# Kernel tuning notes

Measured on AMD Instinct MI355X. Metric: run time of the kernel, lower is better.

## Reference

```python
import jax, jax.numpy as jnp
import numpy as np

KS = 7
HEADS = 8


def _conv1x1(a, w, b):
    # a: (B,Cin,H,W), w: (Cout,Cin), b: (Cout,)
    return jnp.einsum('bchw,oc->bohw', a, w) + b[None, :, None, None]


def _unfold2d(a, ks):
    # a: (B,C,Hp,Wp) -> (B,C,H,W,ks,ks) sliding windows, stride 1
    H = a.shape[2] - ks + 1
    W = a.shape[3] - ks + 1
    ii = jnp.arange(H)[:, None] + jnp.arange(ks)[None, :]  # (H,ks)
    jj = jnp.arange(W)[:, None] + jnp.arange(ks)[None, :]  # (W,ks)
    return a[:, :, ii[:, None, :, None], jj[None, :, None, :]]


def setup_inputs() -> dict:
    key = jax.random.key(0)
    ks = jax.random.split(key, 10)
    B, C, H, W = 4, 128, 56, 56
    x = jax.random.normal(ks[0], (B, C, H, W), dtype=jnp.float32)
    sc = 1.0 / np.sqrt(C)
    q_w = jax.random.normal(ks[1], (C, C), dtype=jnp.float32) * sc
    q_b = jax.random.normal(ks[2], (C,), dtype=jnp.float32) * 0.01
    k_w = jax.random.normal(ks[3], (C, C), dtype=jnp.float32) * sc
    k_b = jax.random.normal(ks[4], (C,), dtype=jnp.float32) * 0.01
    v_w = jax.random.normal(ks[5], (C, C), dtype=jnp.float32) * sc
    v_b = jax.random.normal(ks[6], (C,), dtype=jnp.float32) * 0.01
    rel_h = jax.random.normal(ks[7], (C // 2, KS, 1), dtype=jnp.float32)
    rel_w = jax.random.normal(ks[8], (C // 2, 1, KS), dtype=jnp.float32)
    return {'x': x, 'q_w': q_w, 'q_b': q_b, 'k_w': k_w, 'k_b': k_b,
            'v_w': v_w, 'v_b': v_b, 'rel_h': rel_h, 'rel_w': rel_w}


def reference(x, q_w, q_b, k_w, k_b, v_w, v_b, rel_h, rel_w):
    B, C, H, W = x.shape
    dkh = C // HEADS
    K2 = KS * KS
    pl = (KS - 1) // 2
    pr = KS - 1 - pl
    xp = jnp.pad(x, ((0, 0), (0, 0), (pl, pr), (pl, pr)))

    k = _conv1x1(xp, k_w, k_b)
    v = _conv1x1(xp, v_w, v_b)
    q = _conv1x1(x, q_w, q_b)

    # unfold K/V into (B,C,H,W,KS,KS) then reshape exactly as torch does
    # (this reshape intermixes channel/window axes; replicated faithfully)
    k6 = _unfold2d(k, KS).reshape(B, HEADS, H, W, dkh, K2)
    v6 = _unfold2d(v, KS).reshape(B, HEADS, H, W, dkh, K2)
    q6 = q.reshape(B, HEADS, H, W, dkh, 1)

    # q^T k over the dkh axis -> (B,heads,H,W,KS,KS)
    qk = jnp.einsum('bhxyd,bhxydk->bhxyk', q6[..., 0], k6)
    qk = qk.reshape(B, HEADS, H, W, KS, KS)

    # einsum 'bhxydz,cij->bhxyij' has no shared index: factorizes as
    # (sum over d,z of q) * (sum over c of rel)
    qsum = q6.sum(axis=(4, 5))  # (B,heads,H,W)
    qk = qk + qsum[..., None, None] * rel_h.sum(axis=0)  # (KS,1) broadcast
    qk = qk + qsum[..., None, None] * rel_w.sum(axis=0)  # (1,KS) broadcast

    w = jax.nn.softmax(qk.reshape(B, HEADS, H, W, K2), axis=-1)
    out = jnp.einsum('bhxyk,bhxydk->bhxyd', w, v6)  # (B,heads,H,W,dvh)
    return out.reshape(B, C, H, W)
```

## Files before the change

kernel.cpp:

```cpp
#include <hip/hip_runtime.h>
#include <hip/hip_bf16.h>
#include <math.h>

#define NB    4
#define NC    128
#define NPIX  3136
#define CHW   401408
#define SKS   68

typedef _Float16 f16;
typedef _Float16 f16x8 __attribute__((ext_vector_type(8)));
typedef float f32x4 __attribute__((ext_vector_type(4)));

template <int CTRL, int RM>
__device__ __forceinline__ float dpp_mov(float x, float old) {
    return __int_as_float(__builtin_amdgcn_update_dpp(
        __float_as_int(old), __float_as_int(x), CTRL, RM, 0xf, false));
}
__device__ __forceinline__ float wave_sum(float x) {
    x = x + dpp_mov<0x111, 0xf>(x, 0.f);
    x = x + dpp_mov<0x112, 0xf>(x, 0.f);
    x = x + dpp_mov<0x114, 0xf>(x, 0.f);
    x = x + dpp_mov<0x118, 0xf>(x, 0.f);
    x = x + dpp_mov<0x142, 0xa>(x, 0.f);
    x = x + dpp_mov<0x143, 0xc>(x, 0.f);
    return __int_as_float(__builtin_amdgcn_readlane(__float_as_int(x), 63));
}

__global__ __launch_bounds__(256) void prep_kernel(
    const float* __restrict__ qw, const float* __restrict__ kw,
    const float* __restrict__ vw,
    const float* __restrict__ rel_h, const float* __restrict__ rel_w,
    ushort* __restrict__ pk, float* __restrict__ rb)
{
    int idx = blockIdx.x * 256 + threadIdx.x;
    if (idx < 3 * 32768) {
        int e    = idx & 7;
        int l    = (idx >> 3) & 63;
        int ks   = (idx >> 9) & 3;
        int mt   = (idx >> 11) & 7;
        int prec = (idx >> 14) & 1;
        int mat  = idx >> 15;
        int o = mt * 16 + (l & 15);
        int c = ks * 32 + (l >> 4) * 8 + e;
        const float* src = (mat == 0) ? qw : (mat == 1) ? kw : vw;
        float w = src[o * 128 + c];
        f16 wh = (f16)w;
        f16 v = prec ? (f16)(w - (float)wh) : wh;
        ushort u;
        __builtin_memcpy(&u, &v, 2);
        pk[idx] = u;
    }
    if (idx < 14) {
        const float* src = (idx < 7) ? rel_h : rel_w;
        int off = (idx < 7) ? idx : idx - 7;
        float s = 0.f;
        for (int c = 0; c < 64; ++c) s += src[c * 7 + off];
        rb[idx] = s;
    }
}

__global__ __launch_bounds__(256) void conv_kernel(
    const float* __restrict__ x, const ushort* __restrict__ pk,
    const float* __restrict__ qb, const float* __restrict__ kb,
    const float* __restrict__ vb,
    float* __restrict__ q, float* __restrict__ kbuf, float* __restrict__ vbuf)
{
    __shared__ __align__(16) ushort sh[16 * 136];
    __shared__ __align__(16) ushort sl[16 * 136];
    int bid = blockIdx.x;
    int mat = bid % 3;
    int t2 = bid / 3;
    int tile = t2 % 196;
    int b = t2 / 196;
    int pix0 = tile * 16;
    const float* xb = x + b * CHW + pix0;

    {
        int c = threadIdx.x >> 1;
        int px8 = (threadIdx.x & 1) * 8;
        float4 v0 = *(const float4*)(xb + c * NPIX + px8);
        float4 v1 = *(const float4*)(xb + c * NPIX + px8 + 4);
        float vv[8] = {v0.x, v0.y, v0.z, v0.w, v1.x, v1.y, v1.z, v1.w};
        #pragma unroll
        for (int j = 0; j < 8; ++j) {
            f16 h = (f16)vv[j];
            f16 l = (f16)(vv[j] - (float)h);
            ushort uh, ul;
            __builtin_memcpy(&uh, &h, 2);
            __builtin_memcpy(&ul, &l, 2);
            sh[(px8 + j) * 136 + c] = uh;
            sl[(px8 + j) * 136 + c] = ul;
        }
    }
    __syncthreads();

    int lane = threadIdx.x & 63;
    int wave = threadIdx.x >> 6;
    int px = lane & 15;
    int lg = lane >> 4;

    f16x8 bxh[4], bxl[4];
    #pragma unroll
    for (int ks = 0; ks < 4; ++ks) {
        bxh[ks] = *(const f16x8*)(sh + px * 136 + ks * 32 + lg * 8);
        bxl[ks] = *(const f16x8*)(sl + px * 136 + ks * 32 + lg * 8);
    }

    int mtb = wave * 2;
    const f16x8* PK = (const f16x8*)pk;
    f32x4 acc0 = {0.f, 0.f, 0.f, 0.f};
    f32x4 acc1 = {0.f, 0.f, 0.f, 0.f};
    #pragma unroll
    for (int ks = 0; ks < 4; ++ks) {
        f16x8 wh0 = PK[(((mat * 2 + 0) * 8 + mtb)     * 4 + ks) * 64 + lane];
        f16x8 wh1 = PK[(((mat * 2 + 0) * 8 + mtb + 1) * 4 + ks) * 64 + lane];
        acc0 = __builtin_amdgcn_mfma_f32_16x16x32_f16(wh0, bxh[ks], acc0, 0, 0, 0);
        acc1 = __builtin_amdgcn_mfma_f32_16x16x32_f16(wh1, bxh[ks], acc1, 0, 0, 0);
        acc0 = __builtin_amdgcn_mfma_f32_16x16x32_f16(wh0, bxl[ks], acc0, 0, 0, 0);
        acc1 = __builtin_amdgcn_mfma_f32_16x16x32_f16(wh1, bxl[ks], acc1, 0, 0, 0);
    }
    const float* bias = (mat == 0) ? qb : (mat == 1) ? kb : vb;
    float* dst = ((mat == 0) ? q : (mat == 1) ? kbuf : vbuf)
                 + b * CHW + pix0 + px;
    #pragma unroll
    for (int r = 0; r < 4; ++r) {
        int o0 = mtb * 16 + lg * 4 + r;
        int o1 = o0 + 16;
        dst[o0 * NPIX] = acc0[r] + bias[o0];
        dst[o1 * NPIX] = acc1[r] + bias[o1];
    }
}

__global__ __launch_bounds__(256) void attn_kernel(
    const float* __restrict__ q, const float* __restrict__ kbuf,
    const float* __restrict__ vbuf,
    const float* __restrict__ kb, const float* __restrict__ vb,
    const float* __restrict__ rb, float* __restrict__ out)
{
    __shared__ float sK[20 * SKS];
    __shared__ float sV[21 * SKS];
    __shared__ float sW[4 * 64];
    int bid = blockIdx.x;
    int qpart = bid & 3;
    int bc = bid >> 2;
    int ch = bc & 127;
    const float* qc = q + bc * NPIX + 784 * qpart;
    const float* kc = kbuf + bc * NPIX;
    const float* vc = vbuf + bc * NPIX;
    float* oc = out + bc * NPIX + 784 * qpart;
    float kbias = kb[ch], vbias = vb[ch];
    int qr0 = 14 * qpart;

    for (int i = threadIdx.x; i < 20 * 62; i += 256) {
        int yy = i / 62, xx = i - yy * 62;
        int gy = qr0 + yy - 3;
        int gx = xx - 3;
        bool in = (gy >= 0) && (gy < 56) && (gx >= 0) && (gx < 56);
        int off = in ? gy * 56 + gx : 0;
        float kv = in ? kc[off] : kbias;
        float vv = in ? vc[off] : vbias;
        sK[yy * SKS + xx] = kv;
        sV[yy * SKS + xx] = vv;
    }
    for (int i = threadIdx.x; i < SKS; i += 256) sV[20 * SKS + i] = 0.f;

    int lane = threadIdx.x & 63;
    int wave = threadIdx.x >> 6;
    int k2 = min(lane, 48);
    int di = k2 / 7, dj = k2 - di * 7;
    float rbias = rb[di] + rb[7 + dj];
    int koff = di * SKS + dj;
    int t16 = lane & 15, p = lane >> 4;
    float* sWw = sW + wave * 64;

    float rhM = rb[0], rhm = rb[0];
    #pragma unroll
    for (int i = 1; i < 7; ++i) { rhM = fmaxf(rhM, rb[i]); rhm = fminf(rhm, rb[i]); }
    float rwM = rb[7], rwm = rb[7];
    #pragma unroll
    for (int i = 8; i < 14; ++i) { rwM = fmaxf(rwM, rb[i]); rwm = fminf(rwm, rb[i]); }
    float rdMax = rbias - (rhM + rwM);
    float rdMin = rbias - (rhm + rwm);

    int ul0 = wave * 16;
    int y0 = 0, x0 = ul0;
    float4 p0 = *(const float4*)(qc + ul0);
    float4 p1 = *(const float4*)(qc + ul0 + 4);
    float4 p2 = *(const float4*)(qc + ul0 + 8);
    float4 p3 = *(const float4*)(qc + ul0 + 12);
    __syncthreads();

    for (int gl = wave; gl < 49; gl += 4) {
        float qs = (((p0.x + p0.y) + (p0.z + p0.w)) + ((p1.x + p1.y) + (p1.z + p1.w)))
                 + (((p2.x + p2.y) + (p2.z + p2.w)) + ((p3.x + p3.y) + (p3.z + p3.w)));
        const float* kp = sK + y0 * SKS + x0 + koff;
        int d2 = (x0 == 48) ? (SKS - 48) : 8;
        const float* kp2 = kp + d2;
        float a0, a1;
        a0  = p0.x * kp[0];   a1  = p0.y * kp[1];
        a0 += p0.z * kp[2];   a1 += p0.w * kp[3];
        a0 += p1.x * kp[4];   a1 += p1.y * kp[5];
        a0 += p1.z * kp[6];   a1 += p1.w * kp[7];
        a0 += p2.x * kp2[0];  a1 += p2.y * kp2[1];
        a0 += p2.z * kp2[2];  a1 += p2.w * kp2[3];
        a0 += p3.x * kp2[4];  a1 += p3.y * kp2[5];
        a0 += p3.z * kp2[6];  a1 += p3.w * kp2[7];
        float acc = a0 + a1;

        if (gl + 4 < 49) {
            int un = ul0 + 64;
            p0 = *(const float4*)(qc + un);
            p1 = *(const float4*)(qc + un + 4);
            p2 = *(const float4*)(qc + un + 8);
            p3 = *(const float4*)(qc + un + 12);
        }

        float rd = (qs > 0.f) ? rdMax : rdMin;
        float ex = fmaf(qs, rd, acc);
        float e = (lane < 49) ? __expf(ex) : 0.f;
        float sS = wave_sum(e);
        float wgt = e * __builtin_amdgcn_rcpf(sS);
        sWw[lane] = wgt;

        int u = ul0 + t16;
        int yt = u / 56;
        int xt = u - yt * 56;
        const float* vbase = sV + yt * SKS + xt + p * (2 * SKS);
        const float* wbase = sWw + p * 14;
        float o0 = 0.f, o1 = 0.f;
        #pragma unroll
        for (int j = 0; j < 7; ++j) o0 += wbase[j] * vbase[j];
        #pragma unroll
        for (int j = 0; j < 7; ++j) o1 += wbase[7 + j] * vbase[SKS + j];
        float oacc = o0 + o1;
        oacc += __shfl_xor(oacc, 16);
        oacc += __shfl_xor(oacc, 32);
        if (lane < 16) oc[ul0 + lane] = oacc;

        ul0 += 64;
        x0 += 8; y0 += 1;
        if (x0 >= 56) { x0 -= 56; ++y0; }
    }
}

extern "C" void kernel_launch(void* const* d_in, const int* in_sizes, int n_in,
                              void* d_out, int out_size, void* d_ws, size_t ws_size,
                              hipStream_t stream) {
    const float* x     = (const float*)d_in[0];
    const float* qw    = (const float*)d_in[1];
    const float* qb    = (const float*)d_in[2];
    const float* kw    = (const float*)d_in[3];
    const float* kb    = (const float*)d_in[4];
    const float* vw    = (const float*)d_in[5];
    const float* vb    = (const float*)d_in[6];
    const float* rel_h = (const float*)d_in[7];
    const float* rel_w = (const float*)d_in[8];
    float* out = (float*)d_out;

    float* ws   = (float*)d_ws;
    float* kbuf = ws;
    float* vbuf = kbuf + 1605632;
    float* qbuf = vbuf + 1605632;
    ushort* pk  = (ushort*)(qbuf + 1605632);
    float* rb   = qbuf + 1605632 + 49152;

    prep_kernel<<<384, 256, 0, stream>>>(qw, kw, vw, rel_h, rel_w, pk, rb);
    conv_kernel<<<2352, 256, 0, stream>>>(x, pk, qb, kb, vb,
                                          qbuf, kbuf, vbuf);
    attn_kernel<<<2048, 256, 0, stream>>>(qbuf, kbuf, vbuf, kb, vb, rb, out);
}
```

Baseline: 61.65 us.

## Store V in a bias-padded 64-wide layout and read it directly from global

The conv kernel now writes V into a padded per-channel buffer (62 rows by 64 columns, plus offset) whose border is pre-filled with the V bias by the prep kernel. The attention kernel drops the shared-memory V tile and its staging loop, and instead loads the 7x2 V window for each lane straight from global or cache into registers before the softmax. The lane mapping is changed to put the four partial sums in adjacent lanes, so DPP quad swizzles replace two shuffles. This removes LDS traffic and a staging pass, but adds more scattered global loads and a larger prep launch that fills the padding.

```diff
diff --git a/kernel.cpp b/kernel.cpp
--- a/kernel.cpp
+++ b/kernel.cpp
@@ -6,6 +6,7 @@
 #define NC    128
 #define NPIX  3136
 #define CHW   401408
+#define KVP   3968
 #define SKS   68
 
 typedef _Float16 f16;
@@ -29,11 +30,30 @@
 
 __global__ __launch_bounds__(256) void prep_kernel(
     const float* __restrict__ qw, const float* __restrict__ kw,
-    const float* __restrict__ vw,
+    const float* __restrict__ vw, const float* __restrict__ vb,
     const float* __restrict__ rel_h, const float* __restrict__ rel_w,
-    ushort* __restrict__ pk, float* __restrict__ rb)
+    ushort* __restrict__ pk, float* __restrict__ vpad, float* __restrict__ rb)
 {
     int idx = blockIdx.x * 256 + threadIdx.x;
+    {
+        int img = idx / 708;
+        int hl = idx - img * 708;
+        int p;
+        if (hl < 186) {
+            int r = hl / 62;
+            p = r * 64 + (hl - r * 62);
+        } else if (hl < 372) {
+            int j = hl - 186;
+            int r = j / 62;
+            p = (59 + r) * 64 + (j - r * 62);
+        } else {
+            int j = hl - 372;
+            int r = j / 6, cc = j - r * 6;
+            p = (r + 3) * 64 + (cc < 3 ? cc : cc + 56);
+        }
+        int ch = img & 127;
+        vpad[(size_t)img * KVP + p] = vb[ch];
+    }
     if (idx < 3 * 32768) {
         int e    = idx & 7;
         int l    = (idx >> 3) & 63;
@@ -64,7 +84,7 @@
     const float* __restrict__ x, const ushort* __restrict__ pk,
     const float* __restrict__ qb, const float* __restrict__ kb,
     const float* __restrict__ vb,
-    float* __restrict__ q, float* __restrict__ kbuf, float* __restrict__ vbuf)
+    float* __restrict__ q, float* __restrict__ kbuf, float* __restrict__ vpad)
 {
     __shared__ __align__(16) ushort sh[16 * 136];
     __shared__ __align__(16) ushort sl[16 * 136];
@@ -121,25 +141,34 @@
         acc1 = __builtin_amdgcn_mfma_f32_16x16x32_f16(wh1, bxl[ks], acc1, 0, 0, 0);
     }
     const float* bias = (mat == 0) ? qb : (mat == 1) ? kb : vb;
-    float* dst = ((mat == 0) ? q : (mat == 1) ? kbuf : vbuf)
-                 + b * CHW + pix0 + px;
+    int pp = pix0 + px;
+    int yy = pp / 56, xx = pp - yy * 56;
+    int po = (yy + 3) * 64 + xx + 3;
     #pragma unroll
     for (int r = 0; r < 4; ++r) {
         int o0 = mtb * 16 + lg * 4 + r;
         int o1 = o0 + 16;
-        dst[o0 * NPIX] = acc0[r] + bias[o0];
-        dst[o1 * NPIX] = acc1[r] + bias[o1];
+        float v0 = acc0[r] + bias[o0];
+        float v1 = acc1[r] + bias[o1];
+        if (mat == 2) {
+            float* vd = vpad + (size_t)b * 128 * KVP + po;
+            vd[(size_t)o0 * KVP] = v0;
+            vd[(size_t)o1 * KVP] = v1;
+        } else {
+            float* dst = ((mat == 0) ? q : kbuf) + b * CHW + pix0 + px;
+            dst[o0 * NPIX] = v0;
+            dst[o1 * NPIX] = v1;
+        }
     }
 }
 
 __global__ __launch_bounds__(256) void attn_kernel(
     const float* __restrict__ q, const float* __restrict__ kbuf,
-    const float* __restrict__ vbuf,
-    const float* __restrict__ kb, const float* __restrict__ vb,
-    const float* __restrict__ rb, float* __restrict__ out)
+    const float* __restrict__ vpad,
+    const float* __restrict__ kb, const float* __restrict__ rb,
+    float* __restrict__ out)
 {
     __shared__ float sK[20 * SKS];
-    __shared__ float sV[21 * SKS];
     __shared__ float sW[4 * 64];
     int bid = blockIdx.x;
     int qpart = bid & 3;
@@ -147,10 +176,10 @@
     int ch = bc & 127;
     const float* qc = q + bc * NPIX + 784 * qpart;
     const float* kc = kbuf + bc * NPIX;
-    const float* vc = vbuf + bc * NPIX;
+    int qr0 = 14 * qpart;
+    const float* vq = vpad + (size_t)bc * KVP + qr0 * 64;
     float* oc = out + bc * NPIX + 784 * qpart;
-    float kbias = kb[ch], vbias = vb[ch];
-    int qr0 = 14 * qpart;
+    float kbias = kb[ch];
 
     for (int i = threadIdx.x; i < 20 * 62; i += 256) {
         int yy = i / 62, xx = i - yy * 62;
@@ -158,12 +187,8 @@
         int gx = xx - 3;
         bool in = (gy >= 0) && (gy < 56) && (gx >= 0) && (gx < 56);
         int off = in ? gy * 56 + gx : 0;
-        float kv = in ? kc[off] : kbias;
-        float vv = in ? vc[off] : vbias;
-        sK[yy * SKS + xx] = kv;
-        sV[yy * SKS + xx] = vv;
-    }
-    for (int i = threadIdx.x; i < SKS; i += 256) sV[20 * SKS + i] = 0.f;
+        sK[yy * SKS + xx] = in ? kc[off] : kbias;
+    }
 
     int lane = threadIdx.x & 63;
     int wave = threadIdx.x >> 6;
@@ -171,7 +196,7 @@
     int di = k2 / 7, dj = k2 - di * 7;
     float rbias = rb[di] + rb[7 + dj];
     int koff = di * SKS + dj;
-    int t16 = lane & 15, p = lane >> 4;
+    int t16 = lane >> 2, p = lane & 3;
     float* sWw = sW + wave * 64;
 
     float rhM = rb[0], rhm = rb[0];
@@ -192,6 +217,16 @@
     __syncthreads();
 
     for (int gl = wave; gl < 49; gl += 4) {
+        int ut = ul0 + t16;
+        int ytv = ut / 56;
+        int xtv = ut - ytv * 56;
+        const float* vg = vq + (ytv + 2 * p) * 64 + xtv;
+        float pv0[7], pv1[7];
+        #pragma unroll
+        for (int j = 0; j < 7; ++j) pv0[j] = vg[j];
+        #pragma unroll
+        for (int j = 0; j < 7; ++j) pv1[j] = vg[64 + j];
+
         float qs = (((p0.x + p0.y) + (p0.z + p0.w)) + ((p1.x + p1.y) + (p1.z + p1.w)))
                  + (((p2.x + p2.y) + (p2.z + p2.w)) + ((p3.x + p3.y) + (p3.z + p3.w)));
         const float* kp = sK + y0 * SKS + x0 + koff;
@@ -223,20 +258,16 @@
         float wgt = e * __builtin_amdgcn_rcpf(sS);
         sWw[lane] = wgt;
 
-        int u = ul0 + t16;
-        int yt = u / 56;
-        int xt = u - yt * 56;
-        const float* vbase = sV + yt * SKS + xt + p * (2 * SKS);
         const float* wbase = sWw + p * 14;
         float o0 = 0.f, o1 = 0.f;
         #pragma unroll
-        for (int j = 0; j < 7; ++j) o0 += wbase[j] * vbase[j];
-        #pragma unroll
-        for (int j = 0; j < 7; ++j) o1 += wbase[7 + j] * vbase[SKS + j];
+        for (int j = 0; j < 7; ++j) o0 += wbase[j] * pv0[j];
+        #pragma unroll
+        for (int j = 0; j < 7; ++j) o1 += wbase[7 + j] * pv1[j];
         float oacc = o0 + o1;
-        oacc += __shfl_xor(oacc, 16);
-        oacc += __shfl_xor(oacc, 32);
-        if (lane < 16) oc[ul0 + lane] = oacc;
+        oacc += dpp_mov<0xB1, 0xf>(oacc, 0.f);
+        oacc += dpp_mov<0x4E, 0xf>(oacc, 0.f);
+        if ((lane & 3) == 0) oc[ul0 + (lane >> 2)] = oacc;
 
         ul0 += 64;
         x0 += 8; y0 += 1;
@@ -259,14 +290,15 @@
     float* out = (float*)d_out;
 
     float* ws   = (float*)d_ws;
-    float* kbuf = ws;
-    float* vbuf = kbuf + 1605632;
-    float* qbuf = vbuf + 1605632;
+    float* vpad = ws;
+    float* kbuf = vpad + 2031616;
+    float* qbuf = kbuf + 1605632;
     ushort* pk  = (ushort*)(qbuf + 1605632);
     float* rb   = qbuf + 1605632 + 49152;
 
-    prep_kernel<<<384, 256, 0, stream>>>(qw, kw, vw, rel_h, rel_w, pk, rb);
+    prep_kernel<<<1416, 256, 0, stream>>>(qw, kw, vw, vb, rel_h, rel_w,
+                                          pk, vpad, rb);
     conv_kernel<<<2352, 256, 0, stream>>>(x, pk, qb, kb, vb,
-                                          qbuf, kbuf, vbuf);
-    attn_kernel<<<2048, 256, 0, stream>>>(qbuf, kbuf, vbuf, kb, vb, rb, out);
-}
+                                          qbuf, kbuf, vpad);
+    attn_kernel<<<2048, 256, 0, stream>>>(qbuf, kbuf, vpad, kb, rb, out);
+}
```

Measured after the change: 82.44 us. 1.34x slower.
